# Performance work log

Measured on AMD Instinct MI355X. Metric: run time of the kernel, lower is better.

Reference implementation:

```python
import jax, jax.numpy as jnp
import numpy as np

N = 8192
F_IN = 256
F_OUT = 64
ALPHA = 0.2  # leaky relu negative slope
NEG_BIG = -9e15


def _xavier_uniform(key, shape, gain=1.414):
    fan_in, fan_out = shape[0], shape[1]
    bound = gain * np.sqrt(6.0 / (fan_in + fan_out))
    return jax.random.uniform(key, shape, jnp.float32, -bound, bound)


def setup_inputs() -> dict:
    key = jax.random.key(0)
    k = jax.random.split(key, 6)
    x = jax.random.normal(k[0], (N, F_IN), jnp.float32)
    adj_in = jax.random.randint(k[1], (N, N), 0, 2).astype(jnp.int32)
    adj_out = jax.random.randint(k[2], (N, N), 0, 2).astype(jnp.int32)
    W_in = _xavier_uniform(k[3], (F_IN, F_OUT))
    W_out = _xavier_uniform(k[4], (F_IN, F_OUT))
    a = _xavier_uniform(k[5], (2 * F_OUT, 1))
    return {"x": x, "adj_in": adj_in, "adj_out": adj_out,
            "W_in": W_in, "W_out": W_out, "a": a}


def _gat_branch(h, adj, a):
    # scores: cat([h_i, h_j]) @ a == (h @ a_src)_i + (h @ a_dst)_j
    a_src = a[:F_OUT, 0]   # (F_OUT,)
    a_dst = a[F_OUT:, 0]   # (F_OUT,)
    e = jax.nn.leaky_relu((h @ a_src)[:, None] + (h @ a_dst)[None, :], ALPHA)  # (N, N)
    e = jnp.where(adj > 0, e, jnp.float32(NEG_BIG))
    att = jax.nn.softmax(e, axis=1)
    return att @ h  # (N, F_OUT)


def reference(x, adj_in, adj_out, W_in, W_out, a):
    h_in = x @ W_in
    h_out = x @ W_out
    h_prime_in = _gat_branch(h_in, adj_in, a)
    h_prime_out = _gat_branch(h_out, adj_out, a)
    h_prime = (h_prime_in + h_prime_out) * 0.5
    return jax.nn.elu(h_prime)  # concat=True path
```

## Files before the change

kernel.cpp:

```cpp
#include <hip/hip_runtime.h>
#include <hip/hip_bf16.h>
#include <stdint.h>


#define NN 8192
#define ALPHA 0.2f
#define L2E 1.44269504088896f

typedef _Float16 f16;
typedef _Float16 f16x4 __attribute__((ext_vector_type(4)));
typedef _Float16 f16x8 __attribute__((ext_vector_type(8)));
typedef float f32x4 __attribute__((ext_vector_type(4)));

#define WS_WT    0u
#define WS_HT    65536u
#define WS_SRC   2162688u
#define WS_DST   2228224u
#define WS_DMAX  2293760u
#define WS_PACC  2294016u

__global__ __launch_bounds__(256) void k1_wt(const float* __restrict__ Win,
                                             const float* __restrict__ Wout,
                                             f16* __restrict__ WT) {
    int c = blockIdx.x;
    int k = threadIdx.x;
    const float* W = (c < 64) ? Win : Wout;
    int cc = c & 63;
    WT[(size_t)c * 256 + k] = (f16)W[(size_t)k * 64 + cc];
}

__global__ __launch_bounds__(64) void k2_h(const float* __restrict__ x,
                                           const f16* __restrict__ WT,
                                           const float* __restrict__ a,
                                           f16* __restrict__ HT,
                                           float* __restrict__ srcw,
                                           float* __restrict__ dstw) {
    int l = threadIdx.x;
    int l15 = l & 15, lhi = l >> 4;
    int row0 = blockIdx.x * 16;

    f32x4 acc[8];
#pragma unroll
    for (int n = 0; n < 8; n++) { acc[n][0]=0.f; acc[n][1]=0.f; acc[n][2]=0.f; acc[n][3]=0.f; }

#pragma unroll
    for (int kc = 0; kc < 8; kc++) {
        int k = kc * 32 + lhi * 8;
        const float* xp = x + (size_t)(row0 + l15) * 256 + k;
        float4 xa = *(const float4*)xp;
        float4 xb = *(const float4*)(xp + 4);
        f16x8 af;
        af[0]=(f16)xa.x; af[1]=(f16)xa.y; af[2]=(f16)xa.z; af[3]=(f16)xa.w;
        af[4]=(f16)xb.x; af[5]=(f16)xb.y; af[6]=(f16)xb.z; af[7]=(f16)xb.w;
#pragma unroll
        for (int n = 0; n < 8; n++) {
            f16x8 bf = *(const f16x8*)(WT + (size_t)(16 * n + l15) * 256 + k);
            acc[n] = __builtin_amdgcn_mfma_f32_16x16x32_f16(af, bf, acc[n], 0, 0, 0);
        }
    }

    float as4[4], ad4[4];
#pragma unroll
    for (int nn = 0; nn < 4; nn++) {
        as4[nn] = a[16 * nn + l15];
        ad4[nn] = a[64 + 16 * nn + l15];
    }

    float s_in[4] = {0,0,0,0}, d_in[4] = {0,0,0,0};
    float s_out[4] = {0,0,0,0}, d_out[4] = {0,0,0,0};

#pragma unroll
    for (int n = 0; n < 8; n++) {
        int b = n >> 2;
        int ci = 16 * (n & 3) + l15;
        f16x4 hv;
#pragma unroll
        for (int q = 0; q < 4; q++) hv[q] = (f16)acc[n][q];
        *(f16x4*)(HT + (size_t)b * 524288 + (size_t)ci * 8192 + row0 + 4 * lhi) = hv;
#pragma unroll
        for (int q = 0; q < 4; q++) {
            float v = acc[n][q];
            if (b == 0) { s_in[q]  += v * as4[n & 3]; d_in[q]  += v * ad4[n & 3]; }
            else        { s_out[q] += v * as4[n & 3]; d_out[q] += v * ad4[n & 3]; }
        }
    }

#pragma unroll
    for (int q = 0; q < 4; q++) {
#pragma unroll
        for (int m = 1; m < 16; m <<= 1) {
            s_in[q]  += __shfl_xor(s_in[q],  m, 64);
            d_in[q]  += __shfl_xor(d_in[q],  m, 64);
            s_out[q] += __shfl_xor(s_out[q], m, 64);
            d_out[q] += __shfl_xor(d_out[q], m, 64);
        }
    }
    if (l15 == 0) {
        int row = row0 + 4 * lhi;
#pragma unroll
        for (int q = 0; q < 4; q++) {
            srcw[row + q]        = s_in[q];
            srcw[8192 + row + q] = s_out[q];
            dstw[row + q]        = d_in[q];
            dstw[8192 + row + q] = d_out[q];
        }
    }
}

__global__ __launch_bounds__(256) void k3_dmax(const float* __restrict__ dstw,
                                               float* __restrict__ dmax) {
    __shared__ float red[2][4];
    int t = threadIdx.x;
    int l = t & 63, w = t >> 6;
    for (int b = 0; b < 2; b++) {
        float v = -1e30f;
        for (int i = t; i < 8192; i += 256) v = fmaxf(v, dstw[b * 8192 + i]);
#pragma unroll
        for (int m = 1; m < 64; m <<= 1) v = fmaxf(v, __shfl_xor(v, m, 64));
        if (l == 0) red[b][w] = v;
    }
    __syncthreads();
    if (t == 0) dmax[0] = fmaxf(fmaxf(red[0][0], red[0][1]), fmaxf(red[0][2], red[0][3]));
    if (t == 1) dmax[1] = fmaxf(fmaxf(red[1][0], red[1][1]), fmaxf(red[1][2], red[1][3]));
}

__global__ __launch_bounds__(256) void k4_main(const int* __restrict__ adj_in,
                                               const int* __restrict__ adj_out,
                                               const f16* __restrict__ HT,
                                               const float* __restrict__ srcw,
                                               const float* __restrict__ dstw,
                                               const float* __restrict__ dmaxp,
                                               float* __restrict__ pacc) {
    __shared__ f16 Wlds[16 * 72];
    __shared__ f16 HTlds[64 * 72];
    __shared__ float dsL[2][64];
    __shared__ float dnl[16][17];
    __shared__ float dnr[16];

    int t = threadIdx.x;
    int branch = blockIdx.x & 1;
    int row0 = (blockIdx.x >> 1) * 16;
    const int* adj = branch ? adj_out : adj_in;
    const f16* htg = HT + (size_t)branch * 524288;
    const float* srcb = srcw + branch * 8192;
    const float* dstb = dstw + branch * 8192;
    float dmaxv = dmaxp[branch];

    int r = t & 15, g = t >> 4;
    float srcv = srcb[row0 + r];
    float md = srcv + dmaxv;
    float mlog = fmaxf(md, ALPHA * md) * L2E;
    float srcL = srcv * L2E;

    int l = t & 63, wv = t >> 6;
    int l15 = l & 15, lhi = l >> 4;

    f32x4 acc; acc[0]=0.f; acc[1]=0.f; acc[2]=0.f; acc[3]=0.f;
    float dn = 0.f;

    if (t < 64) dsL[0][t] = dstb[t] * L2E;
    const int* adjrow = adj + (size_t)(row0 + r) * 8192 + 4 * g;
    int4 adjcur = *(const int4*)(adjrow);
    __syncthreads();

    for (int s = 0; s < 128; s++) {
        int j0 = s * 64;
        int snext = (s < 127) ? s + 1 : s;
        int4 adjnext = *(const int4*)(adjrow + (size_t)snext * 64);

        f16x8 h0 = *(const f16x8*)(htg + (size_t)(t >> 3) * 8192 + j0 + (t & 7) * 8);
        f16x8 h1 = *(const f16x8*)(htg + (size_t)((t + 256) >> 3) * 8192 + j0 + (t & 7) * 8);

        if (t < 64) dsL[(s + 1) & 1][t] = dstb[(size_t)snext * 64 + t] * L2E;

        {
            float4 dv = *(const float4*)&dsL[s & 1][4 * g];
            const float* dvp = (const float*)&dv;
            const int* ap = (const int*)&adjcur;
            f16x4 wq;
#pragma unroll
            for (int jj = 0; jj < 4; jj++) {
                float xp = srcL + dvp[jj];
                float lr = fmaxf(xp, ALPHA * xp);
                float e = exp2f(lr - mlog);
                e = (ap[jj] > 0) ? e : 0.f;
                dn += e;
                wq[jj] = (f16)e;
            }
            *(f16x4*)(Wlds + r * 72 + 4 * g) = wq;
        }

        *(f16x8*)(HTlds + (size_t)(t >> 3) * 72 + (t & 7) * 8) = h0;
        *(f16x8*)(HTlds + (size_t)((t + 256) >> 3) * 72 + (t & 7) * 8) = h1;
        __syncthreads();

#pragma unroll
        for (int kc = 0; kc < 2; kc++) {
            f16x8 af = *(const f16x8*)(Wlds + l15 * 72 + kc * 32 + lhi * 8);
            f16x8 bf = *(const f16x8*)(HTlds + (16 * wv + l15) * 72 + kc * 32 + lhi * 8);
            acc = __builtin_amdgcn_mfma_f32_16x16x32_f16(af, bf, acc, 0, 0, 0);
        }
        __syncthreads();
        adjcur = adjnext;
    }

    dnl[r][g] = dn;
    __syncthreads();
    if (t < 16) {
        float sum = 0.f;
#pragma unroll
        for (int gg = 0; gg < 16; gg++) sum += dnl[t][gg];
        dnr[t] = 1.0f / sum;
    }
    __syncthreads();

    float* pb = pacc + (size_t)branch * 524288 + (size_t)row0 * 64;
#pragma unroll
    for (int q = 0; q < 4; q++) {
        int rr = 4 * lhi + q;
        pb[(size_t)rr * 64 + 16 * wv + l15] = acc[q] * dnr[rr];
    }
}

__global__ __launch_bounds__(256) void k5_combine(const float* __restrict__ pacc,
                                                  float* __restrict__ out) {
    size_t idx = (size_t)blockIdx.x * 256 + threadIdx.x;
    float4 p0 = *(const float4*)(pacc + idx * 4);
    float4 p1 = *(const float4*)(pacc + 524288 + idx * 4);
    float4 o;
    float v;
    v = 0.5f * (p0.x + p1.x); o.x = (v > 0.f) ? v : (exp2f(v * L2E) - 1.f);
    v = 0.5f * (p0.y + p1.y); o.y = (v > 0.f) ? v : (exp2f(v * L2E) - 1.f);
    v = 0.5f * (p0.z + p1.z); o.z = (v > 0.f) ? v : (exp2f(v * L2E) - 1.f);
    v = 0.5f * (p0.w + p1.w); o.w = (v > 0.f) ? v : (exp2f(v * L2E) - 1.f);
    *(float4*)(out + idx * 4) = o;
}

extern "C" void kernel_launch(void* const* d_in, const int* in_sizes, int n_in,
                              void* d_out, int out_size, void* d_ws, size_t ws_size,
                              hipStream_t stream) {
    const float* x       = (const float*)d_in[0];
    const int*   adj_in  = (const int*)d_in[1];
    const int*   adj_out = (const int*)d_in[2];
    const float* W_in    = (const float*)d_in[3];
    const float* W_out   = (const float*)d_in[4];
    const float* a       = (const float*)d_in[5];
    float* out = (float*)d_out;

    char* ws = (char*)d_ws;
    f16*   WT   = (f16*)(ws + WS_WT);
    f16*   HT   = (f16*)(ws + WS_HT);
    float* srcw = (float*)(ws + WS_SRC);
    float* dstw = (float*)(ws + WS_DST);
    float* dmax = (float*)(ws + WS_DMAX);
    float* pacc = (float*)(ws + WS_PACC);

    hipLaunchKernelGGL(k1_wt,     dim3(128),  dim3(256), 0, stream, W_in, W_out, WT);
    hipLaunchKernelGGL(k2_h,      dim3(512),  dim3(64),  0, stream, x, WT, a, HT, srcw, dstw);
    hipLaunchKernelGGL(k3_dmax,   dim3(1),    dim3(256), 0, stream, dstw, dmax);
    hipLaunchKernelGGL(k4_main,   dim3(1024), dim3(256), 0, stream, adj_in, adj_out, HT, srcw, dstw, dmax, pacc);
    hipLaunchKernelGGL(k5_combine,dim3(512),  dim3(256), 0, stream, pacc, out);
}
```

Before: 191.1 us.

## Split K across waves in attention kernel, feed MFMA directly from registers

The main attention kernel now gives each of the four waves a contiguous quarter of the neighbor dimension. Each wave computes its own attention weights straight into MFMA A-fragments and loads H^T fragments directly from global memory into registers, which removes the per-step LDS staging and both barriers. Partial accumulators and denominators are reduced through LDS at the end, and the leaky-relu exponent is folded into two FMAs plus a max. The change trades more register pressure and uncoalesced strided global loads for fewer synchronizations, and it sets launch bounds to 4 blocks per CU.

```diff
diff --git a/kernel.cpp b/kernel.cpp
--- a/kernel.cpp
+++ b/kernel.cpp
@@ -6,6 +6,7 @@
 #define NN 8192
 #define ALPHA 0.2f
 #define L2E 1.44269504088896f
+#define AL2E 0.288539008177792f
 
 typedef _Float16 f16;
 typedef _Float16 f16x4 __attribute__((ext_vector_type(4)));
@@ -124,17 +125,15 @@
     if (t == 1) dmax[1] = fmaxf(fmaxf(red[1][0], red[1][1]), fmaxf(red[1][2], red[1][3]));
 }
 
-__global__ __launch_bounds__(256) void k4_main(const int* __restrict__ adj_in,
-                                               const int* __restrict__ adj_out,
-                                               const f16* __restrict__ HT,
-                                               const float* __restrict__ srcw,
-                                               const float* __restrict__ dstw,
-                                               const float* __restrict__ dmaxp,
-                                               float* __restrict__ pacc) {
-    __shared__ f16 Wlds[16 * 72];
-    __shared__ f16 HTlds[64 * 72];
-    __shared__ float dsL[2][64];
-    __shared__ float dnl[16][17];
+__global__ __launch_bounds__(256, 4) void k4_main(const int* __restrict__ adj_in,
+                                                  const int* __restrict__ adj_out,
+                                                  const f16* __restrict__ HT,
+                                                  const float* __restrict__ srcw,
+                                                  const float* __restrict__ dstw,
+                                                  const float* __restrict__ dmaxp,
+                                                  float* __restrict__ pacc) {
+    __shared__ float accL[4][16][64];
+    __shared__ float dnp[4][16];
     __shared__ float dnr[16];
 
     int t = threadIdx.x;
@@ -146,80 +145,93 @@
     const float* dstb = dstw + branch * 8192;
     float dmaxv = dmaxp[branch];
 
-    int r = t & 15, g = t >> 4;
-    float srcv = srcb[row0 + r];
+    int l = t & 63, wv = t >> 6;
+    int l15 = l & 15, lhi = l >> 4, kslc = lhi * 8;
+
+    float srcv = srcb[row0 + l15];
     float md = srcv + dmaxv;
     float mlog = fmaxf(md, ALPHA * md) * L2E;
-    float srcL = srcv * L2E;
-
-    int l = t & 63, wv = t >> 6;
-    int l15 = l & 15, lhi = l >> 4;
-
-    f32x4 acc; acc[0]=0.f; acc[1]=0.f; acc[2]=0.f; acc[3]=0.f;
+    float c1 = srcv * L2E - mlog;
+    float c2 = ALPHA * srcv * L2E - mlog;
+
+    int jbase = wv * 2048 + kslc;
+    const int*   arow = adj  + (size_t)(row0 + l15) * 8192 + jbase;
+    const float* drow = dstb + jbase;
+    const f16*   hrow = htg  + (size_t)l15 * 8192 + jbase;
+
+    f32x4 acc[4];
+#pragma unroll
+    for (int n = 0; n < 4; n++) { acc[n][0]=0.f; acc[n][1]=0.f; acc[n][2]=0.f; acc[n][3]=0.f; }
     float dn = 0.f;
 
-    if (t < 64) dsL[0][t] = dstb[t] * L2E;
-    const int* adjrow = adj + (size_t)(row0 + r) * 8192 + 4 * g;
-    int4 adjcur = *(const int4*)(adjrow);
+    int4   aC0 = *(const int4*)(arow);
+    int4   aC1 = *(const int4*)(arow + 4);
+    float4 dC0 = *(const float4*)(drow);
+    float4 dC1 = *(const float4*)(drow + 4);
+    f16x8  bC0 = *(const f16x8*)(hrow);
+    f16x8  bC1 = *(const f16x8*)(hrow + 16 * 8192);
+    f16x8  bC2 = *(const f16x8*)(hrow + 32 * 8192);
+    f16x8  bC3 = *(const f16x8*)(hrow + 48 * 8192);
+
+    for (int s = 0; s < 64; s++) {
+        int off = ((s < 63) ? (s + 1) : s) * 32;
+        int4   aN0 = *(const int4*)(arow + off);
+        int4   aN1 = *(const int4*)(arow + off + 4);
+        float4 dN0 = *(const float4*)(drow + off);
+        float4 dN1 = *(const float4*)(drow + off + 4);
+        f16x8  bN0 = *(const f16x8*)(hrow + off);
+        f16x8  bN1 = *(const f16x8*)(hrow + off + 16 * 8192);
+        f16x8  bN2 = *(const f16x8*)(hrow + off + 32 * 8192);
+        f16x8  bN3 = *(const f16x8*)(hrow + off + 48 * 8192);
+
+        f16x8 af;
+#pragma unroll
+        for (int e = 0; e < 8; e++) {
+            int   av = (e < 4) ? ((const int*)&aC0)[e]   : ((const int*)&aC1)[e - 4];
+            float d  = (e < 4) ? ((const float*)&dC0)[e] : ((const float*)&dC1)[e - 4];
+            float u = fmaf(L2E, d, c1);
+            float v = fmaf(AL2E, d, c2);
+            float ev = exp2f(fmaxf(u, v));
+            ev = (av > 0) ? ev : 0.f;
+            dn += ev;
+            af[e] = (f16)ev;
+        }
+
+        acc[0] = __builtin_amdgcn_mfma_f32_16x16x32_f16(af, bC0, acc[0], 0, 0, 0);
+        acc[1] = __builtin_amdgcn_mfma_f32_16x16x32_f16(af, bC1, acc[1], 0, 0, 0);
+        acc[2] = __builtin_amdgcn_mfma_f32_16x16x32_f16(af, bC2, acc[2], 0, 0, 0);
+        acc[3] = __builtin_amdgcn_mfma_f32_16x16x32_f16(af, bC3, acc[3], 0, 0, 0);
+
+        aC0 = aN0; aC1 = aN1; dC0 = dN0; dC1 = dN1;
+        bC0 = bN0; bC1 = bN1; bC2 = bN2; bC3 = bN3;
+    }
+
+    dn += __shfl_xor(dn, 16, 64);
+    dn += __shfl_xor(dn, 32, 64);
+    if (lhi == 0) dnp[wv][l15] = dn;
+
+#pragma unroll
+    for (int n = 0; n < 4; n++)
+#pragma unroll
+        for (int q = 0; q < 4; q++)
+            accL[wv][4 * lhi + q][16 * n + l15] = acc[n][q];
     __syncthreads();
 
-    for (int s = 0; s < 128; s++) {
-        int j0 = s * 64;
-        int snext = (s < 127) ? s + 1 : s;
-        int4 adjnext = *(const int4*)(adjrow + (size_t)snext * 64);
-
-        f16x8 h0 = *(const f16x8*)(htg + (size_t)(t >> 3) * 8192 + j0 + (t & 7) * 8);
-        f16x8 h1 = *(const f16x8*)(htg + (size_t)((t + 256) >> 3) * 8192 + j0 + (t & 7) * 8);
-
-        if (t < 64) dsL[(s + 1) & 1][t] = dstb[(size_t)snext * 64 + t] * L2E;
-
-        {
-            float4 dv = *(const float4*)&dsL[s & 1][4 * g];
-            const float* dvp = (const float*)&dv;
-            const int* ap = (const int*)&adjcur;
-            f16x4 wq;
-#pragma unroll
-            for (int jj = 0; jj < 4; jj++) {
-                float xp = srcL + dvp[jj];
-                float lr = fmaxf(xp, ALPHA * xp);
-                float e = exp2f(lr - mlog);
-                e = (ap[jj] > 0) ? e : 0.f;
-                dn += e;
-                wq[jj] = (f16)e;
-            }
-            *(f16x4*)(Wlds + r * 72 + 4 * g) = wq;
-        }
-
-        *(f16x8*)(HTlds + (size_t)(t >> 3) * 72 + (t & 7) * 8) = h0;
-        *(f16x8*)(HTlds + (size_t)((t + 256) >> 3) * 72 + (t & 7) * 8) = h1;
-        __syncthreads();
-
-#pragma unroll
-        for (int kc = 0; kc < 2; kc++) {
-            f16x8 af = *(const f16x8*)(Wlds + l15 * 72 + kc * 32 + lhi * 8);
-            f16x8 bf = *(const f16x8*)(HTlds + (16 * wv + l15) * 72 + kc * 32 + lhi * 8);
-            acc = __builtin_amdgcn_mfma_f32_16x16x32_f16(af, bf, acc, 0, 0, 0);
-        }
-        __syncthreads();
-        adjcur = adjnext;
-    }
-
-    dnl[r][g] = dn;
+    if (t < 16) {
+        float s4 = dnp[0][t] + dnp[1][t] + dnp[2][t] + dnp[3][t];
+        dnr[t] = 1.0f / s4;
+    }
     __syncthreads();
-    if (t < 16) {
-        float sum = 0.f;
-#pragma unroll
-        for (int gg = 0; gg < 16; gg++) sum += dnl[t][gg];
-        dnr[t] = 1.0f / sum;
-    }
-    __syncthreads();
-
-    float* pb = pacc + (size_t)branch * 524288 + (size_t)row0 * 64;
-#pragma unroll
-    for (int q = 0; q < 4; q++) {
-        int rr = 4 * lhi + q;
-        pb[(size_t)rr * 64 + 16 * wv + l15] = acc[q] * dnr[rr];
-    }
+
+    int r = t >> 4;
+    int c4 = (t & 15) * 4;
+    float inv = dnr[r];
+    float4 o;
+    o.x = (accL[0][r][c4+0] + accL[1][r][c4+0] + accL[2][r][c4+0] + accL[3][r][c4+0]) * inv;
+    o.y = (accL[0][r][c4+1] + accL[1][r][c4+1] + accL[2][r][c4+1] + accL[3][r][c4+1]) * inv;
+    o.z = (accL[0][r][c4+2] + accL[1][r][c4+2] + accL[2][r][c4+2] + accL[3][r][c4+2]) * inv;
+    o.w = (accL[0][r][c4+3] + accL[1][r][c4+3] + accL[2][r][c4+3] + accL[3][r][c4+3]) * inv;
+    *(float4*)(pacc + (size_t)branch * 524288 + (size_t)(row0 + r) * 64 + c4) = o;
 }
 
 __global__ __launch_bounds__(256) void k5_combine(const float* __restrict__ pacc,
```

New measurement: 244.1 us. 1.28x slower.
